# Kernel optimization log

Hardware: AMD Instinct MI355X
Metric: run time of the kernel (lower is better)

## Reference

```python
import jax, jax.numpy as jnp
import numpy as np

N, D_FEAT, P, E, L, H, D = 20000, 256, 3, 60000, 4, 8, 32  # d = H*D = 256


def _l2norm(x, axis):
    return x / jnp.maximum(jnp.linalg.norm(x, axis=axis, keepdims=True), 1e-12)


def _gru_last_hidden(edata, w_ih, w_hh, b_ih, b_hh):
    # edata: [E, L, d]; torch nn.GRU gate math, return final hidden [E, d]
    d = w_hh.shape[1]
    def step(h, x):
        gi = x @ w_ih.T + b_ih          # [E, 3d]
        gh = h @ w_hh.T + b_hh
        i_r, i_z, i_n = jnp.split(gi, 3, axis=-1)
        h_r, h_z, h_n = jnp.split(gh, 3, axis=-1)
        r = jax.nn.sigmoid(i_r + h_r)
        z = jax.nn.sigmoid(i_z + h_z)
        n = jnp.tanh(i_n + r * h_n)
        return (1.0 - z) * n + z * h, None
    h0 = jnp.zeros((edata.shape[0], d), edata.dtype)
    h, _ = jax.lax.scan(step, h0, jnp.swapaxes(edata, 0, 1))
    return h


def setup_inputs() -> dict:
    key = jax.random.key(0)
    ks = jax.random.split(key, 10)
    d = H * D
    s = 1.0 / np.sqrt(d)
    return {
        "features": jax.random.normal(ks[0], (N, D_FEAT), jnp.float32),
        "gru_w_ih": jax.random.uniform(ks[1], (P, 3 * d, d), jnp.float32, -s, s),
        "gru_w_hh": jax.random.uniform(ks[2], (P, 3 * d, d), jnp.float32, -s, s),
        "gru_b_ih": jax.random.uniform(ks[3], (P, 3 * d), jnp.float32, -s, s),
        "gru_b_hh": jax.random.uniform(ks[4], (P, 3 * d), jnp.float32, -s, s),
        "fc1_w": jax.random.normal(ks[5], (D, D), jnp.float32) * (1.414 / np.sqrt(D)),
        "fc2": jax.random.normal(ks[6], (H, D), jnp.float32) * (1.414 / np.sqrt(D)),
        "edge_metapath_indices": jax.random.randint(ks[7], (P, E, L), 0, N),
        "edge_dst": jax.random.randint(ks[8], (P, E), 0, N),
    }


def reference(features, gru_w_ih, gru_w_hh, gru_b_ih, gru_b_hh, fc1_w, fc2,
              edge_metapath_indices, edge_dst):
    # node features, normalized across heads (F.normalize default dim=1)
    ft = _l2norm(features.reshape(N, H, D), axis=1)          # [N, H, D]
    metapath_outs = []
    for p in range(P):  # small fixed loop over structurally distinct metapaths
        edata = features[edge_metapath_indices[p]]           # [E, L, d] gather
        hidden = _gru_last_hidden(edata, gru_w_ih[p], gru_w_hh[p],
                                  gru_b_ih[p], gru_b_hh[p])  # [E, d]
        eft = _l2norm(hidden.reshape(E, H, D), axis=1)       # [E, H, D]
        dst = edge_dst[p]                                    # [E]
        sim = jnp.sum(eft * ft[dst], axis=-1)                # [E, H]
        a = jax.nn.softmax(sim, axis=-1)[..., None]          # softmax over heads (faithful)
        nft = jax.ops.segment_sum(eft * a, dst, num_segments=N)  # [N, H, D]
        metapath_outs.append(nft)
    h = jnp.stack(metapath_outs, axis=0)                     # [P, N, H, D]
    # semantic attention across metapaths: fc1 (no bias) then fc2 scoring
    s = jnp.mean(jnp.sum(jnp.tanh(jnp.einsum('pnhd,ed->pnhe', h, fc1_w)) * fc2,
                         axis=(2, 3)), axis=1)               # [P]
    beta = jax.nn.softmax(s)
    out = jnp.einsum('p,pnhd->nhd', beta, h).reshape(N, H * D)
    return out
```

## Files before the change

kernel.cpp:

```cpp
#include <hip/hip_runtime.h>
#include <math.h>


typedef unsigned short u16;
typedef unsigned int u32;
typedef __bf16 bf16x8 __attribute__((ext_vector_type(8)));
typedef short short8 __attribute__((ext_vector_type(8)));
typedef float f32x4 __attribute__((ext_vector_type(4)));

#define N_NODES 20000
#define P_META 3
#define E_EDGES 60000
#define L_STEPS 4
#define DMODEL 256
#define G3 768
#define M_TILE 32
#define TILES_PER_P 1875
#define G_TILES 313

__device__ __forceinline__ float bf2f(u16 b) {
  u32 u = ((u32)b) << 16; float f; __builtin_memcpy(&f, &u, 4); return f;
}
__device__ __forceinline__ u16 f2bf(float f) {
  u32 u; __builtin_memcpy(&u, &f, 4);
  return (u16)((u + 0x7FFFu + ((u >> 16) & 1u)) >> 16);
}
__device__ __forceinline__ u16 f2h(float f) {
  _Float16 h = (_Float16)f; u16 u; __builtin_memcpy(&u, &h, 2); return u;
}
__device__ __forceinline__ float h2f(u16 u) {
  _Float16 h; __builtin_memcpy(&h, &u, 2); return (float)h;
}
__device__ __forceinline__ short8 load8(const void* base, int isbf, size_t off) {
  if (isbf) return *(const short8*)((const u16*)base + off);
  const float* f = (const float*)base + off;
  const float4 a = *(const float4*)f;
  const float4 b = *(const float4*)(f + 4);
  short8 r;
  r[0] = (short)f2bf(a.x); r[1] = (short)f2bf(a.y);
  r[2] = (short)f2bf(a.z); r[3] = (short)f2bf(a.w);
  r[4] = (short)f2bf(b.x); r[5] = (short)f2bf(b.y);
  r[6] = (short)f2bf(b.z); r[7] = (short)f2bf(b.w);
  return r;
}
__device__ __forceinline__ float loadS(const void* base, int isbf, size_t off) {
  return isbf ? bf2f(((const u16*)base)[off]) : ((const float*)base)[off];
}
static __device__ __forceinline__ f32x4 mfma16(short8 a, short8 b, f32x4 c) {
  return __builtin_amdgcn_mfma_f32_16x16x32_bf16(
      __builtin_bit_cast(bf16x8, a), __builtin_bit_cast(bf16x8, b), c, 0, 0, 0);
}
__device__ __forceinline__ float sigm(float x) { return 1.0f / (1.0f + __expf(-x)); }
__device__ __forceinline__ float ftanh(float x) { return 1.0f - 2.0f / (__expf(2.0f * x) + 1.0f); }

__global__ void sniff_kernel(const void* __restrict__ feat, int* __restrict__ flag) {
  const int i = threadIdx.x;
  const u16 e = ((const u16*)feat)[2 * i];
  const int ex = (e >> 7) & 0xFF;
  const bool sane = (e == 0) || (ex >= 103 && ex <= 143);
  const unsigned long long b = __ballot(sane);
  if (i == 0) *flag = (__popcll(b) >= 32) ? 1 : 0;
}

__global__ void pack_weights_kernel(const void* __restrict__ w_ih,
                                    const void* __restrict__ w_hh,
                                    u16* __restrict__ Wpk,
                                    const int* __restrict__ dflag) {
  const int isbf = *dflag;
  const int g = blockIdx.x * 256 + threadIdx.x;
  const int fb = g >> 6, ln = g & 63;
  const int k0 = fb & 7, c = (fb >> 3) & 15, pm = fb >> 7;
  const int p = pm / 6, mat = pm - p * 6;
  const int gate = (mat >= 3) ? mat - 3 : mat;
  const void* W = (mat >= 3) ? w_hh : w_ih;
  const size_t src = ((size_t)p * G3 + gate * 256 + c * 16 + (ln & 15)) * DMODEL
                     + k0 * 32 + (ln >> 4) * 8;
  short8 v = load8(W, isbf, src);
  *(short8*)(Wpk + (size_t)fb * 512 + ln * 8) = v;
}

__global__ void pack_feat_kernel(const void* __restrict__ features,
                                 u16* __restrict__ Fpk,
                                 float* __restrict__ invf,
                                 const int* __restrict__ dflag) {
  const int isbf = *dflag;
  const int n = blockIdx.x * 8 + (threadIdx.x >> 5);
  const int dd = threadIdx.x & 31;
  float v[8]; float ss = 0.f;
  #pragma unroll
  for (int hh = 0; hh < 8; ++hh) {
    v[hh] = loadS(features, isbf, (size_t)n * DMODEL + hh * 32 + dd);
    ss += v[hh] * v[hh];
  }
  invf[(size_t)n * 32 + dd] = 1.0f / fmaxf(sqrtf(ss), 1e-12f);
  #pragma unroll
  for (int hh = 0; hh < 8; ++hh)
    Fpk[(size_t)n * DMODEL + hh * 32 + dd] = f2bf(v[hh]);
}

__global__ void pack_bias_kernel(const void* __restrict__ b_ih,
                                 const void* __restrict__ b_hh,
                                 float* __restrict__ bpk,
                                 const int* __restrict__ dflag) {
  const int isbf = *dflag;
  const int g = blockIdx.x * 256 + threadIdx.x;
  const int p = g / 1536, r = g - p * 1536;
  const int gi = r >> 8, j = r & 255;
  const float v = (gi < 3) ? loadS(b_ih, isbf, (size_t)p * G3 + gi * 256 + j)
                           : loadS(b_hh, isbf, (size_t)p * G3 + (gi - 3) * 256 + j);
  bpk[g] = v;
}

__global__ __launch_bounds__(256, 4) void gih_kernel(
    const u16* __restrict__ Fpk, const u16* __restrict__ Wpk,
    const float* __restrict__ bpk, u16* __restrict__ Gpk,
    u16* __restrict__ H1pk, int p0, int multi)
{
  __shared__ u16 Xb[64 * 256];
  __shared__ float Bs[1536];
  const int tid = threadIdx.x;
  const int bx = blockIdx.x;
  int pb = 0, tile = bx;
  if (multi) { pb = bx / G_TILES; tile = bx - pb * G_TILES; }
  const int p = p0 + pb;
  u16* Gp  = Gpk  + (size_t)pb * (size_t)N_NODES * 1024;
  u16* H1p = H1pk + (size_t)pb * (size_t)N_NODES * DMODEL;
  const int r0 = tile * 64;
  const int wv = tid >> 6, ln = tid & 63;
  const int n16 = ln & 15, quad = ln >> 4;
  const int cbase = wv * 4;

  for (int i = tid; i < 1536; i += 256) Bs[i] = bpk[(size_t)p * 1536 + i];

  const int m4 = tid >> 2, seg = tid & 3, swm = m4 & 7;
  {
    int rr = r0 + m4; if (rr >= N_NODES) rr = N_NODES - 1;
    const u16* frp = Fpk + (size_t)rr * DMODEL;
    #pragma unroll
    for (int u = 0; u < 8; ++u) {
      short8 xv = *(const short8*)(frp + (seg * 8 + u) * 8);
      *(short8*)(Xb + m4 * 256 + (((seg * 8 + u) ^ swm) << 3)) = xv;
    }
  }
  __syncthreads();

  #pragma unroll 1
  for (int ci = 0; ci < 4; ++ci) {
    const int c = cbase + ci;
    const f32x4 z4 = {0.f, 0.f, 0.f, 0.f};
    f32x4 aR[4], aZ[4], aN[4];
    #pragma unroll
    for (int rt = 0; rt < 4; ++rt) { aR[rt] = z4; aZ[rt] = z4; aN[rt] = z4; }
    const u16* wb0 = Wpk + ((size_t)(p * 6 * 16 + c) * 8) * 512 + ln * 8;
    #pragma unroll 2
    for (int k0 = 0; k0 < 8; ++k0) {
      const int un = (((k0 * 4 + quad) ^ (n16 & 7)) << 3);
      const u16* xr = Xb + n16 * 256 + un;
      short8 x0 = *(const short8*)(xr);
      short8 x1 = *(const short8*)(xr + 4096);
      short8 x2 = *(const short8*)(xr + 8192);
      short8 x3 = *(const short8*)(xr + 12288);
      const u16* wk = wb0 + k0 * 512;
      short8 b0 = *(const short8*)(wk);
      short8 b1 = *(const short8*)(wk + 65536);
      short8 b2 = *(const short8*)(wk + 131072);
      aR[0] = mfma16(x0, b0, aR[0]); aR[1] = mfma16(x1, b0, aR[1]);
      aR[2] = mfma16(x2, b0, aR[2]); aR[3] = mfma16(x3, b0, aR[3]);
      aZ[0] = mfma16(x0, b1, aZ[0]); aZ[1] = mfma16(x1, b1, aZ[1]);
      aZ[2] = mfma16(x2, b1, aZ[2]); aZ[3] = mfma16(x3, b1, aZ[3]);
      aN[0] = mfma16(x0, b2, aN[0]); aN[1] = mfma16(x1, b2, aN[1]);
      aN[2] = mfma16(x2, b2, aN[2]); aN[3] = mfma16(x3, b2, aN[3]);
    }
    const int j = c * 16 + n16;
    const float br  = Bs[j],        bz  = Bs[256 + j],  bn  = Bs[512 + j];
    const float bhr = Bs[768 + j],  bhz = Bs[1024 + j], bhn = Bs[1280 + j];
    #pragma unroll
    for (int rt = 0; rt < 4; ++rt) {
      #pragma unroll
      for (int i = 0; i < 4; ++i) {
        const int row = r0 + rt * 16 + quad * 4 + i;
        if (row < N_NODES) {
          const float gr = aR[rt][i] + br;
          const float gz = aZ[rt][i] + bz;
          const float gn = aN[rt][i] + bn;
          const float rr = sigm(gr + bhr);
          const float zz = sigm(gz + bhz);
          const float nn = ftanh(gn + rr * bhn);
          const u16 h1 = f2bf((1.0f - zz) * nn);
          uint2 st;
          st.x = (u32)f2h(gr) | ((u32)f2h(gz) << 16);
          st.y = (u32)f2h(gn) | ((u32)h1 << 16);
          *(uint2*)(Gp + (size_t)row * 1024 + j * 4) = st;
          H1p[(size_t)row * DMODEL + j] = h1;
        }
      }
    }
  }
}

__global__ __launch_bounds__(256, 4) void gru2_edge_kernel(
    const u16*  __restrict__ Fpk,
    const u16*  __restrict__ Wpk,
    const u16*  __restrict__ Gpk,
    const u16*  __restrict__ H1pk,
    const float* __restrict__ bpk,
    const float* __restrict__ invf,
    const int*  __restrict__ emi,
    const int*  __restrict__ edst,
    float*      __restrict__ nft,
    int p0, int multi)
{
  __shared__ u16 HH[2][32 * 256];
  __shared__ float Bsh[768];
  __shared__ int emiS[128];
  __shared__ u16 invhs16[32 * 32];
  __shared__ u16 aws16[32 * 8];

  const int tid  = threadIdx.x;
  const int bx   = blockIdx.x;
  int pb = 0, tile = bx;
  if (multi) { pb = bx / TILES_PER_P; tile = bx - pb * TILES_PER_P; }
  const int p = p0 + pb;
  const u16* Gp  = Gpk  + (size_t)pb * (size_t)N_NODES * 1024;
  const u16* H1p = H1pk + (size_t)pb * (size_t)N_NODES * DMODEL;
  const int e0   = tile * M_TILE;
  const int wv   = tid >> 6;
  const int ln   = tid & 63;
  const int n16  = ln & 15;
  const int quad = ln >> 4;
  const int cbase = wv * 4;

  for (int i = tid; i < 768; i += 256) Bsh[i] = bpk[(size_t)p * 1536 + 768 + i];
  if (tid < 128) {
    const int el = tid >> 2, l = tid & 3;
    emiS[tid] = emi[((size_t)p * E_EDGES + e0 + el) * L_STEPS + l];
  }

  {
    const int m8 = tid >> 3, seg = tid & 7, swm = m8 & 7;
    const int f0 = emi[((size_t)p * E_EDGES + e0 + m8) * L_STEPS];
    const u16* hp = H1p + (size_t)f0 * DMODEL;
    #pragma unroll
    for (int t = 0; t < 4; ++t) {
      const int u = seg * 4 + t;
      short8 xv = *(const short8*)(hp + u * 8);
      *(short8*)(&HH[0][m8 * 256 + ((u ^ swm) << 3)]) = xv;
    }
  }

  uint2 gi[8];

  #pragma unroll 1
  for (int step = 1; step < L_STEPS; ++step) {
    __syncthreads();
    const u16* Ard = &HH[(step & 1) ^ 1][0];
    u16*       Bwr = &HH[step & 1][0];

    if (step == 1) {
      #pragma unroll
      for (int rt = 0; rt < 2; ++rt) {
        #pragma unroll
        for (int i = 0; i < 4; ++i) {
          const int mm = rt * 16 + quad * 4 + i;
          const u32 off = (u32)emiS[mm * 4 + 1] * 2048u + (u32)(n16 * 8)
                          + (u32)(cbase * 128);
          gi[rt * 4 + i] = *(const uint2*)((const char*)Gp + off);
        }
      }
    }

    #pragma unroll 1
    for (int ci = 0; ci < 4; ++ci) {
      const int c = cbase + ci;
      const f32x4 z4 = {0.f, 0.f, 0.f, 0.f};
      f32x4 aHR[2], aHZ[2], aHN[2];
      #pragma unroll
      for (int rt = 0; rt < 2; ++rt) { aHR[rt] = z4; aHZ[rt] = z4; aHN[rt] = z4; }
      const u16* wb0 = Wpk + ((size_t)((p * 6 + 3) * 16 + c) * 8) * 512 + ln * 8;
      #pragma unroll 2
      for (int k0 = 0; k0 < 8; ++k0) {
        const int un = (((k0 * 4 + quad) ^ (n16 & 7)) << 3);
        const u16* hr = Ard + n16 * 256 + un;
        short8 hv0 = *(const short8*)(hr);
        short8 hv1 = *(const short8*)(hr + 4096);
        const u16* wk = wb0 + k0 * 512;
        short8 b3 = *(const short8*)(wk);
        short8 b4 = *(const short8*)(wk + 65536);
        short8 b5 = *(const short8*)(wk + 131072);
        aHR[0] = mfma16(hv0, b3, aHR[0]); aHR[1] = mfma16(hv1, b3, aHR[1]);
        aHZ[0] = mfma16(hv0, b4, aHZ[0]); aHZ[1] = mfma16(hv1, b4, aHZ[1]);
        aHN[0] = mfma16(hv0, b5, aHN[0]); aHN[1] = mfma16(hv1, b5, aHN[1]);
      }
      const int j = c * 16 + n16;
      const float bhr = Bsh[j], bhz = Bsh[256 + j], bhn = Bsh[512 + j];
      const int ju = ((j >> 3) << 3), jl = j & 7;
      const int dopref = (ci < 3) || (step < 3);
      const int nstep = (ci < 3) ? step : step + 1;
      const int nc    = (ci < 3) ? c + 1 : cbase;
      #pragma unroll
      for (int rt = 0; rt < 2; ++rt) {
        #pragma unroll
        for (int i = 0; i < 4; ++i) {
          const int v = rt * 4 + i;
          const int mm = rt * 16 + quad * 4 + i;
          const uint2 g = gi[v];
          if (dopref) {
            const u32 off = (u32)emiS[mm * 4 + nstep] * 2048u + (u32)(n16 * 8)
                            + (u32)(nc * 128);
            gi[v] = *(const uint2*)((const char*)Gp + off);
          }
          const float gr = h2f((u16)(g.x & 0xFFFFu));
          const float gz = h2f((u16)(g.x >> 16));
          const float gn = h2f((u16)(g.y & 0xFFFFu));
          const float r  = sigm(gr + aHR[rt][i] + bhr);
          const float z  = sigm(gz + aHZ[rt][i] + bhz);
          const float ng = ftanh(gn + r * (aHN[rt][i] + bhn));
          const int hoff = mm * 256 + (ju ^ ((mm & 7) << 3)) + jl;
          const float hold = bf2f(Ard[hoff]);
          Bwr[hoff] = f2bf((1.0f - z) * ng + z * hold);
        }
      }
    }
  }
  __syncthreads();
  const u16* Hf = &HH[1][0];

  const int m = tid >> 3, q = tid & 7;
  const int dstn = edst[(size_t)p * E_EDGES + e0 + m];

  ushort4 hq[8], fq[8];
  #pragma unroll
  for (int hh = 0; hh < 8; ++hh) {
    const int unit = 4 * hh + (q >> 1);
    hq[hh] = *(const ushort4*)(Hf + m * 256 + ((unit ^ (m & 7)) << 3) + (q & 1) * 4);
    fq[hh] = *(const ushort4*)(Fpk + (size_t)dstn * DMODEL + hh * 32 + q * 4);
  }
  const float4 ivf4 = *(const float4*)(invf + (size_t)dstn * 32 + q * 4);
  const float invfv[4] = {ivf4.x, ivf4.y, ivf4.z, ivf4.w};

  float invh[4];
  #pragma unroll
  for (int t = 0; t < 4; ++t) {
    float sh = 0.f;
    #pragma unroll
    for (int hh = 0; hh < 8; ++hh) {
      const u16 hb = (&hq[hh].x)[t];
      const float hv = bf2f(hb);
      sh += hv * hv;
    }
    invh[t] = 1.0f / fmaxf(sqrtf(sh), 1e-12f);
  }
  float sim[8];
  #pragma unroll
  for (int hh = 0; hh < 8; ++hh) {
    float s = 0.f;
    #pragma unroll
    for (int t = 0; t < 4; ++t)
      s += (bf2f((&hq[hh].x)[t]) * invh[t]) * (bf2f((&fq[hh].x)[t]) * invfv[t]);
    sim[hh] = s;
  }
  #pragma unroll
  for (int hh = 0; hh < 8; ++hh) {
    sim[hh] += __shfl_xor(sim[hh], 1, 64);
    sim[hh] += __shfl_xor(sim[hh], 2, 64);
    sim[hh] += __shfl_xor(sim[hh], 4, 64);
  }
  float mx = sim[0];
  #pragma unroll
  for (int hh = 1; hh < 8; ++hh) mx = fmaxf(mx, sim[hh]);
  float aw[8], se = 0.f;
  #pragma unroll
  for (int hh = 0; hh < 8; ++hh) { aw[hh] = __expf(sim[hh] - mx); se += aw[hh]; }
  const float sinv = 1.0f / se;

  #pragma unroll
  for (int t = 0; t < 4; ++t) invhs16[m * 32 + q * 4 + t] = f2h(invh[t]);
  if (q == 0) {
    #pragma unroll
    for (int hh = 0; hh < 8; ++hh) aws16[m * 8 + hh] = f2h(aw[hh] * sinv);
  }
  __syncthreads();

  const int esub = ln >> 4;
  const int li   = ln & 15;
  #pragma unroll
  for (int pp = 0; pp < 2; ++pp) {
    const int em = wv * 8 + pp * 4 + esub;
    const int dn = edst[(size_t)p * E_EDGES + e0 + em];
    float* op = nft + ((size_t)p * N_NODES + dn) * DMODEL;
    const u16* ivh = invhs16 + em * 32;
    const u16* awp = aws16 + em * 8;
    #pragma unroll
    for (int t = 0; t < 16; ++t) {
      const int idx = t * 16 + li;
      const u16 hb = Hf[em * 256 + ((((idx >> 3) ^ (em & 7))) << 3) + (idx & 7)];
      const float val = bf2f(hb) * h2f(ivh[idx & 31]) * h2f(awp[idx >> 5]);
      atomicAdd(op + idx, val);
    }
  }
}

__global__ void semantic_score_kernel(const float* __restrict__ nft,
                                      const void* __restrict__ fc1,
                                      const void* __restrict__ fc2,
                                      float* __restrict__ s_out,
                                      const int* __restrict__ dflag) {
  __shared__ float fc1s[32 * 32];
  __shared__ float fc2s[8 * 32];
  __shared__ float red[4];
  const int isbf = *dflag;
  const int tid = threadIdx.x;
  for (int i = tid; i < 1024; i += 256) fc1s[i] = loadS(fc1, isbf, i);
  for (int i = tid; i < 256; i += 256) fc2s[i] = loadS(fc2, isbf, i);
  __syncthreads();
  const int p = blockIdx.y;
  const int g = blockIdx.x * 256 + tid;
  const int n = g >> 3, hh = g & 7;
  const float* hrow = nft + ((size_t)p * N_NODES + n) * DMODEL + hh * 32;
  float hv[32];
  #pragma unroll
  for (int d4 = 0; d4 < 8; ++d4) {
    const float4 v = *(const float4*)(hrow + d4 * 4);
    hv[d4 * 4 + 0] = v.x; hv[d4 * 4 + 1] = v.y; hv[d4 * 4 + 2] = v.z; hv[d4 * 4 + 3] = v.w;
  }
  float acc = 0.f;
  for (int e = 0; e < 32; ++e) {
    float t = 0.f;
    #pragma unroll
    for (int d = 0; d < 32; ++d) t += hv[d] * fc1s[e * 32 + d];
    acc += tanhf(t) * fc2s[hh * 32 + e];
  }
  #pragma unroll
  for (int o = 32; o > 0; o >>= 1) acc += __shfl_xor(acc, o, 64);
  if ((tid & 63) == 0) red[tid >> 6] = acc;
  __syncthreads();
  if (tid == 0) atomicAdd(&s_out[p], red[0] + red[1] + red[2] + red[3]);
}

__global__ void combine_kernel(const float* __restrict__ nft,
                               const float* __restrict__ s_in,
                               void* __restrict__ out,
                               const int* __restrict__ dflag) {
  const int isbf = *dflag;
  const float inv_n = 1.0f / (float)N_NODES;
  const float s0 = s_in[0] * inv_n, s1 = s_in[1] * inv_n, s2 = s_in[2] * inv_n;
  const float mx = fmaxf(s0, fmaxf(s1, s2));
  const float x0 = __expf(s0 - mx), x1 = __expf(s1 - mx), x2 = __expf(s2 - mx);
  const float inv = 1.0f / (x0 + x1 + x2);
  const float w0 = x0 * inv, w1 = x1 * inv, w2 = x2 * inv;
  const size_t stride = (size_t)N_NODES * DMODEL;
  const size_t idx = ((size_t)blockIdx.x * 256 + threadIdx.x) * 4;
  if (idx >= stride) return;
  const float4 a = *(const float4*)(nft + idx);
  const float4 b = *(const float4*)(nft + stride + idx);
  const float4 c = *(const float4*)(nft + 2 * stride + idx);
  const float o0 = w0 * a.x + w1 * b.x + w2 * c.x;
  const float o1 = w0 * a.y + w1 * b.y + w2 * c.y;
  const float o2 = w0 * a.z + w1 * b.z + w2 * c.z;
  const float o3 = w0 * a.w + w1 * b.w + w2 * c.w;
  if (isbf) {
    ushort4 r; r.x = f2bf(o0); r.y = f2bf(o1); r.z = f2bf(o2); r.w = f2bf(o3);
    *(ushort4*)((u16*)out + idx) = r;
  } else {
    float4 r; r.x = o0; r.y = o1; r.z = o2; r.w = o3;
    *(float4*)((float*)out + idx) = r;
  }
}

__global__ void fill_diag_kernel(u16* __restrict__ out, int n) {
  int i = (blockIdx.x * 256 + threadIdx.x) * 8;
  if (i + 8 <= n) {
    const int v = 0x3E003E00;
    int4 w; w.x = v; w.y = v; w.z = v; w.w = v;
    *(int4*)(out + i) = w;
  } else {
    for (; i < n; ++i) out[i] = 0x3E00;
  }
}

extern "C" void kernel_launch(void* const* d_in, const int* in_sizes, int n_in,
                              void* d_out, int out_size, void* d_ws, size_t ws_size,
                              hipStream_t stream) {
  const void* features = d_in[0];
  const void* w_ih     = d_in[1];
  const void* w_hh     = d_in[2];
  const void* b_ih     = d_in[3];
  const void* b_hh     = d_in[4];
  const void* fc1      = d_in[5];
  const void* fc2      = d_in[6];
  const int*  emi      = (const int*)d_in[7];
  const int*  edst     = (const int*)d_in[8];

  const size_t NFT_F   = (size_t)P_META * N_NODES * DMODEL;
  const size_t OFF_WPK = NFT_F + 8;
  const size_t OFF_FPK = OFF_WPK + 589824;
  const size_t OFF_INV = OFF_FPK + 2560000;
  const size_t OFF_BPK = OFF_INV + 640000;
  const size_t OFF_GPK = OFF_BPK + 4608;
  const size_t GPK_PF  = (size_t)N_NODES * 1024 / 2;
  const size_t H1_PF   = (size_t)N_NODES * DMODEL / 2;
  const size_t OFF_H1_FULL = OFF_GPK + 3 * GPK_PF;
  const size_t NEED_FULL   = (OFF_H1_FULL + 3 * H1_PF) * sizeof(float);
  const size_t OFF_H1_LOOP = OFF_GPK + GPK_PF;
  const size_t NEED_LOOP   = (OFF_H1_LOOP + H1_PF) * sizeof(float);

  if (ws_size < NEED_LOOP) {
    fill_diag_kernel<<<dim3((out_size / 8 + 255) / 256), 256, 0, stream>>>((u16*)d_out, out_size);
    return;
  }
  const int full = (ws_size >= NEED_FULL) ? 1 : 0;

  float* wsf  = (float*)d_ws;
  float* nft  = wsf;
  float* s_ws = wsf + NFT_F;
  int*   flag = (int*)(wsf + NFT_F + 3);
  u16*   Wpk  = (u16*)(wsf + OFF_WPK);
  u16*   Fpk  = (u16*)(wsf + OFF_FPK);
  float* invf = wsf + OFF_INV;
  float* bpk  = wsf + OFF_BPK;
  u16*   Gpk  = (u16*)(wsf + OFF_GPK);
  u16*   H1pk = (u16*)(wsf + (full ? OFF_H1_FULL : OFF_H1_LOOP));

  hipMemsetAsync(d_ws, 0, (NFT_F + 8) * sizeof(float), stream);
  sniff_kernel<<<1, 64, 0, stream>>>(features, flag);
  pack_weights_kernel<<<dim3(576), 256, 0, stream>>>(w_ih, w_hh, Wpk, flag);
  pack_feat_kernel<<<dim3(2500), 256, 0, stream>>>(features, Fpk, invf, flag);
  pack_bias_kernel<<<dim3(18), 256, 0, stream>>>(b_ih, b_hh, bpk, flag);
  if (full) {
    gih_kernel<<<dim3(P_META * G_TILES), 256, 0, stream>>>(Fpk, Wpk, bpk, Gpk, H1pk, 0, 1);
    gru2_edge_kernel<<<dim3(P_META * TILES_PER_P), 256, 0, stream>>>(
        Fpk, Wpk, Gpk, H1pk, bpk, invf, emi, edst, nft, 0, 1);
  } else {
    for (int p = 0; p < P_META; ++p) {
      gih_kernel<<<dim3(G_TILES), 256, 0, stream>>>(Fpk, Wpk, bpk, Gpk, H1pk, p, 0);
      gru2_edge_kernel<<<dim3(TILES_PER_P), 256, 0, stream>>>(
          Fpk, Wpk, Gpk, H1pk, bpk, invf, emi, edst, nft, p, 0);
    }
  }
  semantic_score_kernel<<<dim3(625, 3), 256, 0, stream>>>(nft, fc1, fc2, s_ws, flag);
  combine_kernel<<<dim3(5000), 256, 0, stream>>>(nft, s_ws, d_out, flag);
}
```

Before: 736.8 us.

## Double GRU edge tile to 64 edges with 512 threads and prefold r/z biases

Raises the edge tile in the recurrent GRU kernel from 32 to 64 edges, using 512 threads (8 waves). Each wave now covers 2 column chunks over 4 row tiles, so every loaded W_hh fragment feeds twice as many MFMAs and weight traffic per edge drops. The hidden-state r and z biases are folded into the precomputed input gates in gih_kernel, leaving only the n-gate bias in shared memory. Because 60000 is not a multiple of 64, edge indices are clamped and out-of-range atomics skipped. The larger block also doubles LDS per block, which can reduce occupancy, and storing the folded sums in fp16 adds some rounding.

```diff
diff --git a/kernel.cpp b/kernel.cpp
--- a/kernel.cpp
+++ b/kernel.cpp
@@ -14,8 +14,8 @@
 #define L_STEPS 4
 #define DMODEL 256
 #define G3 768
-#define M_TILE 32
-#define TILES_PER_P 1875
+#define M_TILE 64
+#define TILES_PER_P 938
 #define G_TILES 313
 
 __device__ __forceinline__ float bf2f(u16 b) {
@@ -180,15 +180,15 @@
       for (int i = 0; i < 4; ++i) {
         const int row = r0 + rt * 16 + quad * 4 + i;
         if (row < N_NODES) {
-          const float gr = aR[rt][i] + br;
-          const float gz = aZ[rt][i] + bz;
-          const float gn = aN[rt][i] + bn;
-          const float rr = sigm(gr + bhr);
-          const float zz = sigm(gz + bhz);
+          const float grb = aR[rt][i] + br + bhr;
+          const float gzb = aZ[rt][i] + bz + bhz;
+          const float gn  = aN[rt][i] + bn;
+          const float rr = sigm(grb);
+          const float zz = sigm(gzb);
           const float nn = ftanh(gn + rr * bhn);
           const u16 h1 = f2bf((1.0f - zz) * nn);
           uint2 st;
-          st.x = (u32)f2h(gr) | ((u32)f2h(gz) << 16);
+          st.x = (u32)f2h(grb) | ((u32)f2h(gzb) << 16);
           st.y = (u32)f2h(gn) | ((u32)h1 << 16);
           *(uint2*)(Gp + (size_t)row * 1024 + j * 4) = st;
           H1p[(size_t)row * DMODEL + j] = h1;
@@ -198,7 +198,7 @@
   }
 }
 
-__global__ __launch_bounds__(256, 4) void gru2_edge_kernel(
+__global__ __launch_bounds__(512, 4) void gru2_edge_kernel(
     const u16*  __restrict__ Fpk,
     const u16*  __restrict__ Wpk,
     const u16*  __restrict__ Gpk,
@@ -210,11 +210,11 @@
     float*      __restrict__ nft,
     int p0, int multi)
 {
-  __shared__ u16 HH[2][32 * 256];
-  __shared__ float Bsh[768];
-  __shared__ int emiS[128];
-  __shared__ u16 invhs16[32 * 32];
-  __shared__ u16 aws16[32 * 8];
+  __shared__ u16 HH[2][64 * 256];
+  __shared__ float Bsh[256];
+  __shared__ int emiS[256];
+  __shared__ u16 invhs16[64 * 32];
+  __shared__ u16 aws16[64 * 8];
 
   const int tid  = threadIdx.x;
   const int bx   = blockIdx.x;
@@ -228,17 +228,20 @@
   const int ln   = tid & 63;
   const int n16  = ln & 15;
   const int quad = ln >> 4;
-  const int cbase = wv * 4;
-
-  for (int i = tid; i < 768; i += 256) Bsh[i] = bpk[(size_t)p * 1536 + 768 + i];
-  if (tid < 128) {
-    const int el = tid >> 2, l = tid & 3;
-    emiS[tid] = emi[((size_t)p * E_EDGES + e0 + el) * L_STEPS + l];
+  const int cbase = wv * 2;
+
+  if (tid < 256) Bsh[tid] = bpk[(size_t)p * 1536 + 1280 + tid];
+  if (tid >= 256 && tid < 512) {
+    const int t = tid - 256;
+    const int el = t >> 2, l = t & 3;
+    int ec = e0 + el; if (ec >= E_EDGES) ec = E_EDGES - 1;
+    emiS[t] = emi[((size_t)p * E_EDGES + ec) * L_STEPS + l];
   }
 
   {
     const int m8 = tid >> 3, seg = tid & 7, swm = m8 & 7;
-    const int f0 = emi[((size_t)p * E_EDGES + e0 + m8) * L_STEPS];
+    int em8 = e0 + m8; if (em8 >= E_EDGES) em8 = E_EDGES - 1;
+    const int f0 = emi[((size_t)p * E_EDGES + em8) * L_STEPS];
     const u16* hp = H1p + (size_t)f0 * DMODEL;
     #pragma unroll
     for (int t = 0; t < 4; ++t) {
@@ -248,7 +251,7 @@
     }
   }
 
-  uint2 gi[8];
+  uint2 gi[16];
 
   #pragma unroll 1
   for (int step = 1; step < L_STEPS; ++step) {
@@ -258,7 +261,7 @@
 
     if (step == 1) {
       #pragma unroll
-      for (int rt = 0; rt < 2; ++rt) {
+      for (int rt = 0; rt < 4; ++rt) {
         #pragma unroll
         for (int i = 0; i < 4; ++i) {
           const int mm = rt * 16 + quad * 4 + i;
@@ -270,12 +273,12 @@
     }
 
     #pragma unroll 1
-    for (int ci = 0; ci < 4; ++ci) {
+    for (int ci = 0; ci < 2; ++ci) {
       const int c = cbase + ci;
       const f32x4 z4 = {0.f, 0.f, 0.f, 0.f};
-      f32x4 aHR[2], aHZ[2], aHN[2];
+      f32x4 aHR[4], aHZ[4], aHN[4];
       #pragma unroll
-      for (int rt = 0; rt < 2; ++rt) { aHR[rt] = z4; aHZ[rt] = z4; aHN[rt] = z4; }
+      for (int rt = 0; rt < 4; ++rt) { aHR[rt] = z4; aHZ[rt] = z4; aHN[rt] = z4; }
       const u16* wb0 = Wpk + ((size_t)((p * 6 + 3) * 16 + c) * 8) * 512 + ln * 8;
       #pragma unroll 2
       for (int k0 = 0; k0 < 8; ++k0) {
@@ -283,22 +286,27 @@
         const u16* hr = Ard + n16 * 256 + un;
         short8 hv0 = *(const short8*)(hr);
         short8 hv1 = *(const short8*)(hr + 4096);
+        short8 hv2 = *(const short8*)(hr + 8192);
+        short8 hv3 = *(const short8*)(hr + 12288);
         const u16* wk = wb0 + k0 * 512;
         short8 b3 = *(const short8*)(wk);
         short8 b4 = *(const short8*)(wk + 65536);
         short8 b5 = *(const short8*)(wk + 131072);
         aHR[0] = mfma16(hv0, b3, aHR[0]); aHR[1] = mfma16(hv1, b3, aHR[1]);
+        aHR[2] = mfma16(hv2, b3, aHR[2]); aHR[3] = mfma16(hv3, b3, aHR[3]);
         aHZ[0] = mfma16(hv0, b4, aHZ[0]); aHZ[1] = mfma16(hv1, b4, aHZ[1]);
+        aHZ[2] = mfma16(hv2, b4, aHZ[2]); aHZ[3] = mfma16(hv3, b4, aHZ[3]);
         aHN[0] = mfma16(hv0, b5, aHN[0]); aHN[1] = mfma16(hv1, b5, aHN[1]);
+        aHN[2] = mfma16(hv2, b5, aHN[2]); aHN[3] = mfma16(hv3, b5, aHN[3]);
       }
       const int j = c * 16 + n16;
-      const float bhr = Bsh[j], bhz = Bsh[256 + j], bhn = Bsh[512 + j];
+      const float bhn = Bsh[j];
       const int ju = ((j >> 3) << 3), jl = j & 7;
-      const int dopref = (ci < 3) || (step < 3);
-      const int nstep = (ci < 3) ? step : step + 1;
-      const int nc    = (ci < 3) ? c + 1 : cbase;
+      const int dopref = (ci < 1) || (step < 3);
+      const int nstep = (ci < 1) ? step : step + 1;
+      const int nc    = (ci < 1) ? c + 1 : cbase;
       #pragma unroll
-      for (int rt = 0; rt < 2; ++rt) {
+      for (int rt = 0; rt < 4; ++rt) {
         #pragma unroll
         for (int i = 0; i < 4; ++i) {
           const int v = rt * 4 + i;
@@ -309,11 +317,11 @@
                             + (u32)(nc * 128);
             gi[v] = *(const uint2*)((const char*)Gp + off);
           }
-          const float gr = h2f((u16)(g.x & 0xFFFFu));
-          const float gz = h2f((u16)(g.x >> 16));
-          const float gn = h2f((u16)(g.y & 0xFFFFu));
-          const float r  = sigm(gr + aHR[rt][i] + bhr);
-          const float z  = sigm(gz + aHZ[rt][i] + bhz);
+          const float grb = h2f((u16)(g.x & 0xFFFFu));
+          const float gzb = h2f((u16)(g.x >> 16));
+          const float gn  = h2f((u16)(g.y & 0xFFFFu));
+          const float r  = sigm(grb + aHR[rt][i]);
+          const float z  = sigm(gzb + aHZ[rt][i]);
           const float ng = ftanh(gn + r * (aHN[rt][i] + bhn));
           const int hoff = mm * 256 + (ju ^ ((mm & 7) << 3)) + jl;
           const float hold = bf2f(Ard[hoff]);
@@ -326,7 +334,8 @@
   const u16* Hf = &HH[1][0];
 
   const int m = tid >> 3, q = tid & 7;
-  const int dstn = edst[(size_t)p * E_EDGES + e0 + m];
+  int ecl = e0 + m; if (ecl >= E_EDGES) ecl = E_EDGES - 1;
+  const int dstn = edst[(size_t)p * E_EDGES + ecl];
 
   ushort4 hq[8], fq[8];
   #pragma unroll
@@ -344,8 +353,7 @@
     float sh = 0.f;
     #pragma unroll
     for (int hh = 0; hh < 8; ++hh) {
-      const u16 hb = (&hq[hh].x)[t];
-      const float hv = bf2f(hb);
+      const float hv = bf2f((&hq[hh].x)[t]);
       sh += hv * hv;
     }
     invh[t] = 1.0f / fmaxf(sqrtf(sh), 1e-12f);
@@ -386,16 +394,19 @@
   #pragma unroll
   for (int pp = 0; pp < 2; ++pp) {
     const int em = wv * 8 + pp * 4 + esub;
-    const int dn = edst[(size_t)p * E_EDGES + e0 + em];
-    float* op = nft + ((size_t)p * N_NODES + dn) * DMODEL;
-    const u16* ivh = invhs16 + em * 32;
-    const u16* awp = aws16 + em * 8;
-    #pragma unroll
-    for (int t = 0; t < 16; ++t) {
-      const int idx = t * 16 + li;
-      const u16 hb = Hf[em * 256 + ((((idx >> 3) ^ (em & 7))) << 3) + (idx & 7)];
-      const float val = bf2f(hb) * h2f(ivh[idx & 31]) * h2f(awp[idx >> 5]);
-      atomicAdd(op + idx, val);
+    const int ee = e0 + em;
+    if (ee < E_EDGES) {
+      const int dn = edst[(size_t)p * E_EDGES + ee];
+      float* op = nft + ((size_t)p * N_NODES + dn) * DMODEL;
+      const u16* ivh = invhs16 + em * 32;
+      const u16* awp = aws16 + em * 8;
+      #pragma unroll
+      for (int t = 0; t < 16; ++t) {
+        const int idx = t * 16 + li;
+        const u16 hb = Hf[em * 256 + ((((idx >> 3) ^ (em & 7))) << 3) + (idx & 7)];
+        const float val = bf2f(hb) * h2f(ivh[idx & 31]) * h2f(awp[idx >> 5]);
+        atomicAdd(op + idx, val);
+      }
     }
   }
 }
@@ -528,12 +539,12 @@
   pack_bias_kernel<<<dim3(18), 256, 0, stream>>>(b_ih, b_hh, bpk, flag);
   if (full) {
     gih_kernel<<<dim3(P_META * G_TILES), 256, 0, stream>>>(Fpk, Wpk, bpk, Gpk, H1pk, 0, 1);
-    gru2_edge_kernel<<<dim3(P_META * TILES_PER_P), 256, 0, stream>>>(
+    gru2_edge_kernel<<<dim3(P_META * TILES_PER_P), 512, 0, stream>>>(
         Fpk, Wpk, Gpk, H1pk, bpk, invf, emi, edst, nft, 0, 1);
   } else {
     for (int p = 0; p < P_META; ++p) {
       gih_kernel<<<dim3(G_TILES), 256, 0, stream>>>(Fpk, Wpk, bpk, Gpk, H1pk, p, 0);
-      gru2_edge_kernel<<<dim3(TILES_PER_P), 256, 0, stream>>>(
+      gru2_edge_kernel<<<dim3(TILES_PER_P), 512, 0, stream>>>(
           Fpk, Wpk, Gpk, H1pk, bpk, invf, emi, edst, nft, p, 0);
     }
   }
```

After: 1.123 ms. +52.5%, slower.
